# Performance work log

Measured on AMD Instinct MI355X. Metric: run time of the kernel, lower is better.

Reference implementation:

```python
import jax, jax.numpy as jnp
import numpy as np

B, H, C = 131072, 16, 32        # batch, n_holidays, n_changepoints
HID, HP, SKU = 512, 512 // 16, 64  # hidden_dim, hidden per holiday, sku embed dim
TEMP = 0.7
TIME_MAX = 365.0
LN_EPS = 1e-3  # keras LayerNormalization default epsilon


def mish(x):
    return x * jnp.tanh(jax.nn.softplus(x))


def setup_inputs() -> dict:
    key = jax.random.key(0)
    ks = jax.random.split(key, 12)
    inputs = jax.random.uniform(ks[0], (B, H), dtype=jnp.float32) * TIME_MAX
    sku_embedding = jax.random.normal(ks[1], (B, SKU), dtype=jnp.float32)
    # per-holiday params, stacked over holiday axis
    deltas = jnp.full((H, C), TIME_MAX / C, dtype=jnp.float32)  # changepoint_deltas init
    ln_gamma = jnp.ones((H, C), dtype=jnp.float32)
    ln_beta = jnp.zeros((H, C), dtype=jnp.float32)
    attn_w = jax.random.normal(ks[2], (H,), dtype=jnp.float32) * 0.5  # Dense(1) on [...,1]
    Wh = jax.random.normal(ks[3], (H, C, HP), dtype=jnp.float32) * (1.0 / np.sqrt(C))
    Wah = jax.random.normal(ks[4], (HID, HID), dtype=jnp.float32) * (1.0 / np.sqrt(HID))
    Waa = jax.random.normal(ks[5], (HID, HID), dtype=jnp.float32) * (1.0 / np.sqrt(HID))
    Wb = jax.random.normal(ks[6], (SKU, HID), dtype=jnp.float32) * (1.0 / np.sqrt(SKU))
    Wa = jax.random.normal(ks[7], (SKU, HID), dtype=jnp.float32) * (1.0 / np.sqrt(SKU))
    Wo = jax.random.normal(ks[8], (HID, 1), dtype=jnp.float32)
    Wo = Wo / jnp.linalg.norm(Wo, axis=0, keepdims=True)  # UnitNorm(axis=0) constraint
    return {"inputs": inputs, "sku_embedding": sku_embedding, "deltas": deltas,
            "ln_gamma": ln_gamma, "ln_beta": ln_beta, "attn_w": attn_w, "Wh": Wh,
            "Wah": Wah, "Waa": Waa, "Wb": Wb, "Wa": Wa, "Wo": Wo}


def reference(inputs, sku_embedding, deltas, ln_gamma, ln_beta, attn_w, Wh, Wah, Waa, Wb, Wa, Wo):
    # ChangepointReLU (vectorised over holidays): softplus -> cumsum -> rescale to [0, 365]
    pd = jax.nn.softplus(deltas)                     # [H, C]
    cps = jnp.cumsum(pd, axis=-1)
    cps = cps / cps[:, -1:] * TIME_MAX               # time_min = 0
    feats = jax.nn.relu(inputs[:, :, None] - cps[None, :, :])  # [B, H, C]
    # per-holiday LayerNorm over changepoint axis
    mu = jnp.mean(feats, axis=-1, keepdims=True)
    var = jnp.mean((feats - mu) ** 2, axis=-1, keepdims=True)
    normed = (feats - mu) * jax.lax.rsqrt(var + LN_EPS) * ln_gamma[None] + ln_beta[None]
    # per-holiday attention: Dense(1,no bias) on [...,1] == scalar multiply per holiday
    logits = normed * attn_w[None, :, None]
    attn = jax.nn.softmax(logits / TEMP, axis=-1)    # n_changepoints > 1
    attended = normed * attn                          # [B, H, C]
    # per-holiday hidden Dense(HP, mish, no bias), then concat over holidays
    hid = mish(jnp.einsum('bhc,hcd->bhd', attended, Wh))  # [B, H, HP]
    aggregated = hid.reshape(hid.shape[0], H * HP)        # [B, HID]
    agg_hidden = mish(aggregated @ Wah)                   # [B, HID]
    agg_attn = jax.nn.softmax((agg_hidden @ Waa) / TEMP, axis=-1)
    final = agg_hidden * agg_attn                         # dropout inactive (inference)
    beta = jax.nn.sigmoid(sku_embedding @ Wb)
    alpha = sku_embedding @ Wa
    final = final * beta + alpha
    return final @ Wo                                     # [B, 1]
```

## Files before the change

### kernel.cpp

```cpp
#include <hip/hip_runtime.h>
#include <hip/hip_fp16.h>
#include <stdint.h>

#define B_TOT 131072
#define CHUNK 65536
#define NH 16
#define NC 32
#define HIDD 512

typedef unsigned short u16;
typedef __attribute__((ext_vector_type(8))) short short8;
typedef __attribute__((ext_vector_type(4))) float f32x4;
typedef __attribute__((ext_vector_type(4))) int i32x4;

#define GLLDS(g, l) __builtin_amdgcn_global_load_lds((const __attribute__((address_space(1))) unsigned int*)(g), (__attribute__((address_space(3))) unsigned int*)(l), 16, 0, 0)

__device__ __forceinline__ u16 f2bf(float x){
  unsigned u = __float_as_uint(x);
  u += 0x7fffu + ((u >> 16) & 1u);
  return (u16)(u >> 16);
}
__device__ __forceinline__ float bf2f(u16 b){ return __uint_as_float(((unsigned)b) << 16); }
__device__ __forceinline__ u16 f2h(float x){ __half h = __float2half(x); return *(u16*)&h; }
__device__ __forceinline__ float h2f(u16 b){ __half h; *(u16*)&h = b; return __half2float(h); }
__device__ __forceinline__ float mishf(float x){
  float e = __expf(fminf(x, 30.f));
  float u = 1.f + e;
  float u2 = u * u;
  return x * (u2 - 1.f) / (u2 + 1.f);
}

__global__ void prep_small(const float* __restrict__ deltas, const float* __restrict__ Wa,
                           const float* __restrict__ Wo, float* __restrict__ cps, float* __restrict__ wWo)
{
  const int t = threadIdx.x;
  if (t < NH){
    float cum[NC];
    float run = 0.f;
#pragma unroll
    for (int c = 0; c < NC; c++){
      float d = deltas[t*NC + c];
      float sp = (d > 20.f) ? d : log1pf(__expf(d));
      run += sp; cum[c] = run;
    }
    float s = 365.0f / run;
#pragma unroll
    for (int c = 0; c < NC; c++) cps[t*NC + c] = cum[c] * s;
  } else if (t >= 64 && t < 128){
    const int k = t - 64;
    float s = 0.f;
    for (int n = 0; n < HIDD; n++) s += Wa[k*HIDD + n] * Wo[n];
    wWo[k] = s;
  }
}

__global__ void prep_convert(const float* __restrict__ Wah, const float* __restrict__ Waa,
                             const float* __restrict__ Wb, const float* __restrict__ Wh,
                             u16* __restrict__ WahT, u16* __restrict__ WaaT,
                             u16* __restrict__ WbT, u16* __restrict__ WhT)
{
  int i = blockIdx.x * 256 + threadIdx.x;
  if (i < 262144){ int n = i >> 9, k = i & 511; WahT[i] = f2bf(Wah[k*512 + n]); return; }
  i -= 262144;
  if (i < 262144){ int n = i >> 9, k = i & 511; WaaT[i] = f2bf(Waa[k*512 + n]); return; }
  i -= 262144;
  if (i < 32768){ int n = i >> 6, k = i & 63; WbT[i] = f2bf(Wb[k*512 + n]); return; }
  i -= 32768;
  if (i < 16384){ int h = i >> 10, r = i & 1023, d = r >> 5, c = r & 31;
                  WhT[i] = f2bf(Wh[h*1024 + c*32 + d]); return; }
}

__global__ __launch_bounds__(256) void stage1_kernel(
    const float* __restrict__ inputs, const float* __restrict__ sku,
    const float* __restrict__ ln_g, const float* __restrict__ ln_b,
    const float* __restrict__ attnw, const float* __restrict__ cps,
    const float* __restrict__ wWo, const u16* __restrict__ WhT,
    u16* __restrict__ agg, u16* __restrict__ skub, float* __restrict__ skd)
{
  __shared__ __align__(16) float in_l[256];
  __shared__ __align__(16) float cps_l[512];
  __shared__ __align__(16) float gam_l[512];
  __shared__ __align__(16) float bet_l[512];
  __shared__ float aw_l[16];
  __shared__ __align__(16) u16 at_l[16*16*32];
  __shared__ __align__(16) u16 ot_l[16*512];

  const int t = threadIdx.x;
  const int ln = t & 63;
  const long bb = (long)blockIdx.x * 16;

  in_l[t] = inputs[bb*16 + t];
  cps_l[t] = cps[t];       cps_l[t+256] = cps[t+256];
  gam_l[t] = ln_g[t];      gam_l[t+256] = ln_g[t+256];
  bet_l[t] = ln_b[t];      bet_l[t+256] = ln_b[t+256];
  if (t < 16) aw_l[t] = attnw[t];
  {
    const f32x4 sv = *(const f32x4*)&sku[bb*64 + t*4];
    unsigned lo = (unsigned)f2bf(sv.x) | ((unsigned)f2bf(sv.y) << 16);
    unsigned hi = (unsigned)f2bf(sv.z) | ((unsigned)f2bf(sv.w) << 16);
    unsigned long long v = (unsigned long long)lo | ((unsigned long long)hi << 32);
    *(unsigned long long*)&skub[bb*64 + t*4] = v;
    const f32x4 wv4 = *(const f32x4*)&wWo[(ln & 15)*4];
    float pd = sv.x*wv4.x + sv.y*wv4.y + sv.z*wv4.z + sv.w*wv4.w;
#pragma unroll
    for (int s = 1; s < 16; s <<= 1) pd += __shfl_xor(pd, s);
    if ((ln & 15) == 0) skd[bb + (t >> 4)] = pd;
  }
  __syncthreads();

  const int h = t >> 4, bi = t & 15;
  const float x = in_l[bi*16 + h];
  float nrm[NC], pw[NC];
  float s1 = 0.f;
#pragma unroll
  for (int c = 0; c < NC; c++){ float f = fmaxf(x - cps_l[h*NC + c], 0.f); nrm[c] = f; s1 += f; }
  const float mu = s1 * (1.f/NC);
  float s2 = 0.f;
#pragma unroll
  for (int c = 0; c < NC; c++){ float d = nrm[c] - mu; s2 += d*d; }
  const float rs = rsqrtf(s2 * (1.f/NC) + 1e-3f);
  const float aw = aw_l[h] * (1.0f/0.7f);
  float lmax = -1e30f;
#pragma unroll
  for (int c = 0; c < NC; c++){
    float nv = (nrm[c] - mu) * rs * gam_l[h*NC + c] + bet_l[h*NC + c];
    nrm[c] = nv;
    lmax = fmaxf(lmax, nv * aw);
  }
  float ps = 0.f;
#pragma unroll
  for (int c = 0; c < NC; c++){ float p = __expf(nrm[c]*aw - lmax); pw[c] = p; ps += p; }
  const float invs = 1.f / ps;
#pragma unroll
  for (int c = 0; c < NC; c += 2){
    unsigned pk = (unsigned)f2bf(nrm[c]*pw[c]*invs) | ((unsigned)f2bf(nrm[c+1]*pw[c+1]*invs) << 16);
    *(unsigned*)&at_l[h*512 + bi*32 + c] = pk;
  }
  __syncthreads();

  const int wv = t >> 6;
  const int lrow = ln & 15, lq = ln >> 4;
#pragma unroll
  for (int q = 0; q < 4; q++){
    const int hh = wv*4 + q;
    short8 af  = *(const short8*)&at_l[hh*512 + lrow*32 + lq*8];
    short8 bf0 = *(const short8*)&WhT[hh*1024 + lrow*32 + lq*8];
    short8 bf1 = *(const short8*)&WhT[hh*1024 + (16 + lrow)*32 + lq*8];
    f32x4 acc0 = {0.f,0.f,0.f,0.f}, acc1 = {0.f,0.f,0.f,0.f};
    acc0 = __builtin_amdgcn_mfma_f32_16x16x32_bf16(af, bf0, acc0, 0, 0, 0);
    acc1 = __builtin_amdgcn_mfma_f32_16x16x32_bf16(af, bf1, acc1, 0, 0, 0);
#pragma unroll
    for (int r = 0; r < 4; r++){
      const int br = lq*4 + r;
      ot_l[br*512 + hh*32 + lrow]      = f2bf(mishf(acc0[r]));
      ot_l[br*512 + hh*32 + 16 + lrow] = f2bf(mishf(acc1[r]));
    }
  }
  __syncthreads();
  {
    const int row = t >> 4, c16 = t & 15;
    const i32x4* src = (const i32x4*)&ot_l[row*512 + c16*32];
    i32x4* dst = (i32x4*)&agg[(bb + row)*512 + c16*32];
#pragma unroll
    for (int j = 0; j < 4; j++) dst[j] = src[j];
  }
}

__global__ __launch_bounds__(256, 3) void gemm_bw(
    const u16* __restrict__ A, const u16* __restrict__ Bt,
    const float* __restrict__ Wo, u16* __restrict__ bw)
{
  __shared__ __align__(16) u16 As[2][128*32];
  __shared__ __align__(16) u16 Bs[2][128*32];
  const int t = threadIdx.x, wv = t >> 6, ln = t & 63;
  const int g = blockIdx.x;
  const int m_idx = (g & 7) + ((g >> 5) << 3);
  const int n_idx = (g >> 3) & 3;
  const long m0 = (long)m_idx * 128;
  const int n0 = n_idx * 128;
  const int lrow = ln & 15, lq = ln >> 4;
  const int wm = wv >> 1, wn = wv & 1;

  auto stage = [&](int buf, int kt){
#pragma unroll
    for (int p = 0; p < 2; p++){
      const int chunk = p*256 + wv*64 + ln;
      const int mm = chunk >> 2, kc = chunk & 3;
      const int kcl = kc ^ ((mm >> 1) & 3);
      GLLDS(&A[(m0 + mm)*64 + kt + kcl*8],  &As[buf][(p*256 + wv*64)*8]);
      GLLDS(&Bt[(n0 + mm)*64 + kt + kcl*8], &Bs[buf][(p*256 + wv*64)*8]);
    }
  };

  f32x4 acc[4][4] = {};
  stage(0, 0);
  for (int ks = 0; ks < 2; ks++){
    const int cur = ks & 1;
    __syncthreads();
    if (ks + 1 < 2) stage(cur ^ 1, (ks + 1)*32);
    short8 a[4], b[4];
#pragma unroll
    for (int i = 0; i < 4; i++){
      const int ra = wm*64 + i*16 + lrow;
      const int rb = wn*64 + i*16 + lrow;
      const int lqa = lq ^ ((ra >> 1) & 3);
      const int lqb = lq ^ ((rb >> 1) & 3);
      a[i] = *(const short8*)&As[cur][ra*32 + lqa*8];
      b[i] = *(const short8*)&Bs[cur][rb*32 + lqb*8];
    }
#pragma unroll
    for (int i = 0; i < 4; i++)
#pragma unroll
      for (int j = 0; j < 4; j++)
        acc[i][j] = __builtin_amdgcn_mfma_f32_16x16x32_bf16(a[i], b[j], acc[i][j], 0, 0, 0);
  }
#pragma unroll
  for (int j = 0; j < 4; j++){
    const int n = n0 + wn*64 + j*16 + lrow;
    const float wo = Wo[n];
#pragma unroll
    for (int i = 0; i < 4; i++){
#pragma unroll
      for (int r = 0; r < 4; r++){
        const long m = m0 + wm*64 + i*16 + lq*4 + r;
        const float sig = 1.f / (1.f + __expf(-acc[i][j][r]));
        bw[m*512 + n] = f2h(sig * wo);
      }
    }
  }
}

__global__ __launch_bounds__(512, 2) void gemm_mishw(
    const u16* __restrict__ A, const u16* __restrict__ Bt,
    const u16* __restrict__ bw, u16* __restrict__ aggh, u16* __restrict__ wp)
{
  __shared__ __align__(16) u16 As[2][128*32];
  __shared__ __align__(16) u16 Bs[2][512*32];
  const int t = threadIdx.x, wv = t >> 6, ln = t & 63;
  const int lrow = ln & 15, lq = ln >> 4;
  const int rh = wv >> 2, cq = wv & 3;
  const long m0 = (long)blockIdx.x * 128;

  auto stageA = [&](int buf, int kt){
    const int mm = t >> 2, kc = t & 3;
    const int kcl = kc ^ ((mm >> 1) & 3);
    GLLDS(&A[(m0 + mm)*512 + kt + kcl*8], &As[buf][t*8]);
  };
  auto stageB = [&](int buf, int kt){
#pragma unroll
    for (int p = 0; p < 4; p++){
      const int idx = p*512 + t;
      const int mm = idx >> 2, kc = idx & 3;
      const int kcl = kc ^ ((mm >> 1) & 3);
      GLLDS(&Bt[(long)mm*512 + kt + kcl*8], &Bs[buf][idx*8]);
    }
  };

  f32x4 acc[4][8] = {};
  stageA(0, 0); stageB(0, 0);
  for (int ks = 0; ks < 16; ks++){
    const int cur = ks & 1;
    __syncthreads();
    if (ks + 1 < 16){ stageA(cur ^ 1, (ks + 1)*32); stageB(cur ^ 1, (ks + 1)*32); }
    short8 a[4], b[8];
#pragma unroll
    for (int i = 0; i < 4; i++){
      const int ra = rh*64 + i*16 + lrow;
      const int lqa = lq ^ ((ra >> 1) & 3);
      a[i] = *(const short8*)&As[cur][ra*32 + lqa*8];
    }
#pragma unroll
    for (int j = 0; j < 8; j++){
      const int rb = cq*128 + j*16 + lrow;
      const int lqb = lq ^ ((rb >> 1) & 3);
      b[j] = *(const short8*)&Bs[cur][rb*32 + lqb*8];
    }
#pragma unroll
    for (int i = 0; i < 4; i++)
#pragma unroll
      for (int j = 0; j < 8; j++)
        acc[i][j] = __builtin_amdgcn_mfma_f32_16x16x32_bf16(a[i], b[j], acc[i][j], 0, 0, 0);
  }
#pragma unroll
  for (int i = 0; i < 4; i++){
#pragma unroll
    for (int j = 0; j < 8; j++){
#pragma unroll
      for (int r = 0; r < 4; r++){
        const long m = m0 + rh*64 + i*16 + lq*4 + r;
        const int n = cq*128 + j*16 + lrow;
        const float h = mishf(acc[i][j][r]);
        aggh[m*512 + n] = f2bf(h);
        wp[m*512 + n]   = f2h(h * h2f(bw[m*512 + n]));
      }
    }
  }
}

__global__ __launch_bounds__(512, 2) void mega2(
    const u16* __restrict__ A, const u16* __restrict__ Bt,
    const u16* __restrict__ wprod, const float* __restrict__ skd,
    float* __restrict__ outp)
{
  __shared__ __align__(16) u16 As[2][128*32];
  __shared__ __align__(16) u16 Bs[2][512*32];
  const int t = threadIdx.x, wv = t >> 6, ln = t & 63;
  const int lrow = ln & 15, lq = ln >> 4;
  const int rh = wv >> 2, cq = wv & 3;
  const long m0 = (long)blockIdx.x * 128;

  auto stageA = [&](int buf, int kt){
    const int mm = t >> 2, kc = t & 3;
    const int kcl = kc ^ ((mm >> 1) & 3);
    GLLDS(&A[(m0 + mm)*512 + kt + kcl*8], &As[buf][t*8]);
  };
  auto stageB = [&](int buf, int kt){
#pragma unroll
    for (int p = 0; p < 4; p++){
      const int idx = p*512 + t;
      const int mm = idx >> 2, kc = idx & 3;
      const int kcl = kc ^ ((mm >> 1) & 3);
      GLLDS(&Bt[(long)mm*512 + kt + kcl*8], &Bs[buf][idx*8]);
    }
  };

  f32x4 acc[4][8] = {};
  stageA(0, 0); stageB(0, 0);
  for (int ks = 0; ks < 16; ks++){
    const int cur = ks & 1;
    __syncthreads();
    if (ks + 1 < 16){ stageA(cur ^ 1, (ks + 1)*32); stageB(cur ^ 1, (ks + 1)*32); }
    short8 a[4], b[8];
#pragma unroll
    for (int i = 0; i < 4; i++){
      const int ra = rh*64 + i*16 + lrow;
      const int lqa = lq ^ ((ra >> 1) & 3);
      a[i] = *(const short8*)&As[cur][ra*32 + lqa*8];
    }
#pragma unroll
    for (int j = 0; j < 8; j++){
      const int rb = cq*128 + j*16 + lrow;
      const int lqb = lq ^ ((rb >> 1) & 3);
      b[j] = *(const short8*)&Bs[cur][rb*32 + lqb*8];
    }
#pragma unroll
    for (int i = 0; i < 4; i++)
#pragma unroll
      for (int j = 0; j < 8; j++)
        acc[i][j] = __builtin_amdgcn_mfma_f32_16x16x32_bf16(a[i], b[j], acc[i][j], 0, 0, 0);
  }

  __syncthreads();
  float* mxs = (float*)&Bs[0][0];
  float* sss = mxs + 512;
  float* tts = sss + 512;
  const float inv_t = 1.0f / 0.7f;

#pragma unroll
  for (int i = 0; i < 4; i++){
#pragma unroll
    for (int r = 0; r < 4; r++){
      float tm = acc[i][0][r];
#pragma unroll
      for (int j = 1; j < 8; j++) tm = fmaxf(tm, acc[i][j][r]);
#pragma unroll
      for (int s = 1; s < 16; s <<= 1) tm = fmaxf(tm, __shfl_xor(tm, s));
      if (lrow == 0) mxs[(rh*64 + i*16 + lq*4 + r)*4 + cq] = tm;
    }
  }
  __syncthreads();
#pragma unroll
  for (int i = 0; i < 4; i++){
#pragma unroll
    for (int r = 0; r < 4; r++){
      const int row = rh*64 + i*16 + lq*4 + r;
      const float gm = fmaxf(fmaxf(mxs[row*4+0], mxs[row*4+1]),
                             fmaxf(mxs[row*4+2], mxs[row*4+3]));
      float sp = 0.f, tp = 0.f;
#pragma unroll
      for (int j = 0; j < 8; j++){
        const float e = __expf((acc[i][j][r] - gm) * inv_t);
        sp += e;
        tp += e * h2f(wprod[(m0 + row)*512 + cq*128 + j*16 + lrow]);
      }
#pragma unroll
      for (int s = 1; s < 16; s <<= 1){ sp += __shfl_xor(sp, s); tp += __shfl_xor(tp, s); }
      if (lrow == 0){ sss[row*4 + cq] = sp; tts[row*4 + cq] = tp; }
    }
  }
  __syncthreads();
  if (t < 128){
    const float S = sss[t*4] + sss[t*4+1] + sss[t*4+2] + sss[t*4+3];
    const float T = tts[t*4] + tts[t*4+1] + tts[t*4+2] + tts[t*4+3];
    outp[m0 + t] = T / S + skd[m0 + t];
  }
}

__global__ void ws_too_small(float* o, float v){ o[(long)blockIdx.x*256 + threadIdx.x] = v; }

extern "C" void kernel_launch(void* const* d_in, const int* in_sizes, int n_in,
                              void* d_out, int out_size, void* d_ws, size_t ws_size,
                              hipStream_t stream)
{
  const float* inputs = (const float*)d_in[0];
  const float* sku    = (const float*)d_in[1];
  const float* deltas = (const float*)d_in[2];
  const float* ln_g   = (const float*)d_in[3];
  const float* ln_b   = (const float*)d_in[4];
  const float* attnw  = (const float*)d_in[5];
  const float* Wh     = (const float*)d_in[6];
  const float* Wah    = (const float*)d_in[7];
  const float* Waa    = (const float*)d_in[8];
  const float* Wb     = (const float*)d_in[9];
  const float* Wa     = (const float*)d_in[10];
  const float* Wo     = (const float*)d_in[11];
  float* outp = (float*)d_out;

  const size_t OFF_CPS  = 0;
  const size_t OFF_WWO  = 2048;
  const size_t OFF_WAHT = 4096;
  const size_t OFF_WAAT = OFF_WAHT + 524288;
  const size_t OFF_WBT  = OFF_WAAT + 524288;
  const size_t OFF_WHT  = OFF_WBT  + 65536;
  const size_t OFF_SKUB = OFF_WHT  + 32768;
  const size_t OFF_SKD  = OFF_SKUB + (size_t)CHUNK*64*2;
  const size_t OFF_AGG  = OFF_SKD  + (size_t)CHUNK*4;
  const size_t OFF_BW   = OFF_AGG  + (size_t)CHUNK*512*2;
  const size_t OFF_AGH  = OFF_BW   + (size_t)CHUNK*512*2;
  const size_t NEED     = OFF_AGH  + (size_t)CHUNK*512*2;

  if (ws_size < NEED){
    hipLaunchKernelGGL(ws_too_small, dim3(B_TOT/256), dim3(256), 0, stream,
                       outp, -(float)(ws_size >> 20));
    return;
  }

  char* ws = (char*)d_ws;
  float* cps  = (float*)(ws + OFF_CPS);
  float* wWo  = (float*)(ws + OFF_WWO);
  u16* WahT   = (u16*)(ws + OFF_WAHT);
  u16* WaaT   = (u16*)(ws + OFF_WAAT);
  u16* WbT    = (u16*)(ws + OFF_WBT);
  u16* WhT    = (u16*)(ws + OFF_WHT);
  u16* skub   = (u16*)(ws + OFF_SKUB);
  float* skd  = (float*)(ws + OFF_SKD);
  u16* agg    = (u16*)(ws + OFF_AGG);
  u16* bw     = (u16*)(ws + OFF_BW);
  u16* aggh   = (u16*)(ws + OFF_AGH);
  u16* wprod  = agg;

  hipLaunchKernelGGL(prep_small, dim3(1), dim3(128), 0, stream, deltas, Wa, Wo, cps, wWo);
  hipLaunchKernelGGL(prep_convert, dim3(2240), dim3(256), 0, stream,
                     Wah, Waa, Wb, Wh, WahT, WaaT, WbT, WhT);

  for (int ch = 0; ch < B_TOT / CHUNK; ch++){
    const float* in_c  = inputs + (size_t)ch * CHUNK * 16;
    const float* sku_c = sku    + (size_t)ch * CHUNK * 64;
    float* out_c       = outp   + (size_t)ch * CHUNK;

    hipLaunchKernelGGL(stage1_kernel, dim3(CHUNK/16), dim3(256), 0, stream,
                       in_c, sku_c, ln_g, ln_b, attnw, cps, wWo, WhT, agg, skub, skd);
    hipLaunchKernelGGL(gemm_bw, dim3(CHUNK/128*4), dim3(256), 0, stream,
                       skub, WbT, Wo, bw);
    hipLaunchKernelGGL(gemm_mishw, dim3(CHUNK/128), dim3(512), 0, stream,
                       agg, WahT, bw, aggh, wprod);
    hipLaunchKernelGGL(mega2, dim3(CHUNK/128), dim3(512), 0, stream,
                       aggh, WaaT, wprod, skd, out_c);
  }
}
```

Before: 553.8 us.

## Drop wprod intermediate and stage mish epilogue through LDS for coalesced stores

The Wah GEMM epilogue no longer reads bw or writes a separate fp16 product buffer. It now writes mish outputs as bf16 into shared memory and copies them out with 16-byte row-contiguous stores instead of scattered 2-byte stores. The final kernel recomputes the product by reading aggh and bw directly. This removes one full BxHID write and read pair and the uncoalesced epilogue stores. In exchange it adds extra syncs and an LDS pass, and the mega2 epilogue now does scattered reads of two arrays instead of one.

```diff
diff --git a/kernel.cpp b/kernel.cpp
--- a/kernel.cpp
+++ b/kernel.cpp
@@ -230,12 +230,12 @@
   }
 }
 
-__global__ __launch_bounds__(512, 2) void gemm_mishw(
-    const u16* __restrict__ A, const u16* __restrict__ Bt,
-    const u16* __restrict__ bw, u16* __restrict__ aggh, u16* __restrict__ wp)
-{
-  __shared__ __align__(16) u16 As[2][128*32];
-  __shared__ __align__(16) u16 Bs[2][512*32];
+__global__ __launch_bounds__(512, 2) void gemm_mish(
+    const u16* __restrict__ A, const u16* __restrict__ Bt, u16* __restrict__ aggh)
+{
+  __shared__ __align__(16) u16 lds[2*128*32 + 2*512*32];
+  u16* As0 = lds;
+  u16* Bs0 = lds + 2*128*32;
   const int t = threadIdx.x, wv = t >> 6, ln = t & 63;
   const int lrow = ln & 15, lq = ln >> 4;
   const int rh = wv >> 2, cq = wv & 3;
@@ -244,7 +244,7 @@
   auto stageA = [&](int buf, int kt){
     const int mm = t >> 2, kc = t & 3;
     const int kcl = kc ^ ((mm >> 1) & 3);
-    GLLDS(&A[(m0 + mm)*512 + kt + kcl*8], &As[buf][t*8]);
+    GLLDS(&A[(m0 + mm)*512 + kt + kcl*8], &As0[buf*4096 + t*8]);
   };
   auto stageB = [&](int buf, int kt){
 #pragma unroll
@@ -252,7 +252,7 @@
       const int idx = p*512 + t;
       const int mm = idx >> 2, kc = idx & 3;
       const int kcl = kc ^ ((mm >> 1) & 3);
-      GLLDS(&Bt[(long)mm*512 + kt + kcl*8], &Bs[buf][idx*8]);
+      GLLDS(&Bt[(long)mm*512 + kt + kcl*8], &Bs0[buf*16384 + idx*8]);
     }
   };
 
@@ -267,13 +267,13 @@
     for (int i = 0; i < 4; i++){
       const int ra = rh*64 + i*16 + lrow;
       const int lqa = lq ^ ((ra >> 1) & 3);
-      a[i] = *(const short8*)&As[cur][ra*32 + lqa*8];
+      a[i] = *(const short8*)&As0[cur*4096 + ra*32 + lqa*8];
     }
 #pragma unroll
     for (int j = 0; j < 8; j++){
       const int rb = cq*128 + j*16 + lrow;
       const int lqb = lq ^ ((rb >> 1) & 3);
-      b[j] = *(const short8*)&Bs[cur][rb*32 + lqb*8];
+      b[j] = *(const short8*)&Bs0[cur*16384 + rb*32 + lqb*8];
     }
 #pragma unroll
     for (int i = 0; i < 4; i++)
@@ -281,25 +281,35 @@
       for (int j = 0; j < 8; j++)
         acc[i][j] = __builtin_amdgcn_mfma_f32_16x16x32_bf16(a[i], b[j], acc[i][j], 0, 0, 0);
   }
-#pragma unroll
-  for (int i = 0; i < 4; i++){
-#pragma unroll
-    for (int j = 0; j < 8; j++){
-#pragma unroll
-      for (int r = 0; r < 4; r++){
-        const long m = m0 + rh*64 + i*16 + lq*4 + r;
-        const int n = cq*128 + j*16 + lrow;
-        const float h = mishf(acc[i][j][r]);
-        aggh[m*512 + n] = f2bf(h);
-        wp[m*512 + n]   = f2h(h * h2f(bw[m*512 + n]));
-      }
-    }
+
+  const int TP = 528;
+  __syncthreads();
+#pragma unroll 1
+  for (int h = 0; h < 2; h++){
+    if (rh == h){
+#pragma unroll
+      for (int i = 0; i < 4; i++)
+#pragma unroll
+        for (int j = 0; j < 8; j++)
+#pragma unroll
+          for (int r = 0; r < 4; r++)
+            lds[(i*16 + lq*4 + r)*TP + cq*128 + j*16 + lrow] = f2bf(mishf(acc[i][j][r]));
+    }
+    __syncthreads();
+#pragma unroll
+    for (int it = 0; it < 8; it++){
+      const int idx = it*512 + t;
+      const int row = idx >> 6, off = idx & 63;
+      const i32x4 v = *(const i32x4*)&lds[row*TP + off*8];
+      *(i32x4*)&aggh[(m0 + h*64 + row)*512 + off*8] = v;
+    }
+    __syncthreads();
   }
 }
 
 __global__ __launch_bounds__(512, 2) void mega2(
     const u16* __restrict__ A, const u16* __restrict__ Bt,
-    const u16* __restrict__ wprod, const float* __restrict__ skd,
+    const u16* __restrict__ bw, const float* __restrict__ skd,
     float* __restrict__ outp)
 {
   __shared__ __align__(16) u16 As[2][128*32];
@@ -379,9 +389,10 @@
       float sp = 0.f, tp = 0.f;
 #pragma unroll
       for (int j = 0; j < 8; j++){
+        const long gi = (m0 + row)*512 + cq*128 + j*16 + lrow;
         const float e = __expf((acc[i][j][r] - gm) * inv_t);
         sp += e;
-        tp += e * h2f(wprod[(m0 + row)*512 + cq*128 + j*16 + lrow]);
+        tp += e * bf2f(A[gi]) * h2f(bw[gi]);
       }
 #pragma unroll
       for (int s = 1; s < 16; s <<= 1){ sp += __shfl_xor(sp, s); tp += __shfl_xor(tp, s); }
@@ -447,7 +458,6 @@
   u16* agg    = (u16*)(ws + OFF_AGG);
   u16* bw     = (u16*)(ws + OFF_BW);
   u16* aggh   = (u16*)(ws + OFF_AGH);
-  u16* wprod  = agg;
 
   hipLaunchKernelGGL(prep_small, dim3(1), dim3(128), 0, stream, deltas, Wa, Wo, cps, wWo);
   hipLaunchKernelGGL(prep_convert, dim3(2240), dim3(256), 0, stream,
@@ -462,9 +472,9 @@
                        in_c, sku_c, ln_g, ln_b, attnw, cps, wWo, WhT, agg, skub, skd);
     hipLaunchKernelGGL(gemm_bw, dim3(CHUNK/128*4), dim3(256), 0, stream,
                        skub, WbT, Wo, bw);
-    hipLaunchKernelGGL(gemm_mishw, dim3(CHUNK/128), dim3(512), 0, stream,
-                       agg, WahT, bw, aggh, wprod);
+    hipLaunchKernelGGL(gemm_mish, dim3(CHUNK/128), dim3(512), 0, stream,
+                       agg, WahT, aggh);
     hipLaunchKernelGGL(mega2, dim3(CHUNK/128), dim3(512), 0, stream,
-                       aggh, WaaT, wprod, skd, out_c);
-  }
-}
+                       aggh, WaaT, bw, skd, out_c);
+  }
+}
```

New measurement: 520.5 us. 1.06x faster.
